# Performance work log

Hardware: AMD Instinct MI355X
Metric: run time of the kernel (lower is better)

## Reference

```python
import jax, jax.numpy as jnp
import numpy as np
import math

B, S, D, H = 2, 2048, 1024, 16
DH = D // H
MASK_VALUE = -1000000.0  # module uses -1e6, not -inf


def setup_inputs() -> dict:
    key = jax.random.key(0)
    ks = jax.random.split(key, 8)
    scale = 1.0 / math.sqrt(D)
    return {
        "queries": jax.random.normal(ks[0], (B, S, D), jnp.float32),
        "keys": jax.random.normal(ks[1], (B, S, D), jnp.float32),
        "values": jax.random.normal(ks[2], (B, S, D), jnp.float32),
        "valid_lens": jax.random.randint(ks[3], (B,), 1, S + 1, jnp.int32),
        "Wq": jax.random.normal(ks[4], (D, D), jnp.float32) * scale,
        "Wk": jax.random.normal(ks[5], (D, D), jnp.float32) * scale,
        "Wv": jax.random.normal(ks[6], (D, D), jnp.float32) * scale,
        "Wo": jax.random.normal(ks[7], (D, D), jnp.float32) * scale,
    }


def _split_heads(x):
    # [B, S, D] -> [B, H, S, DH]
    b, s, d = x.shape
    return x.reshape(b, s, H, DH).transpose(0, 2, 1, 3)


def reference(queries, keys, values, valid_lens, Wq, Wk, Wv, Wo):
    q = _split_heads(queries @ Wq)          # [B, H, S, DH]
    k = _split_heads(keys @ Wk)
    v = _split_heads(values @ Wv)
    scores = jnp.einsum("bhqd,bhkd->bhqk", q, k) / math.sqrt(DH)
    # valid_lens [B]: one length per batch row, broadcast over heads & queries
    mask = jnp.arange(scores.shape[-1])[None, None, None, :] < valid_lens[:, None, None, None]
    scores = jnp.where(mask, scores, MASK_VALUE)
    attn = jax.nn.softmax(scores, axis=-1)  # dropout is identity in eval
    out = jnp.einsum("bhqk,bhkd->bhqd", attn, v)   # [B, H, S, DH]
    out = out.transpose(0, 2, 1, 3).reshape(queries.shape[0], queries.shape[1], D)
    return out @ Wo
```

## Files before the change

### kernel.cpp

```cpp
#include <hip/hip_runtime.h>
#include <stdint.h>

#define BB 2
#define SS 2048
#define DD 1024
#define HH 16
#define DHD 64
#define MM (BB * SS)

typedef unsigned short u16;
typedef unsigned int u32;
typedef __attribute__((ext_vector_type(8))) short bhalf8;
typedef __attribute__((ext_vector_type(4))) float floatx4;
typedef __attribute__((ext_vector_type(2))) u32 u32x2;
typedef __attribute__((ext_vector_type(4))) u32 u32x4;
typedef __attribute__((address_space(3))) u32 as3_u32;
typedef __attribute__((address_space(1))) u32 as1_u32;

__device__ __forceinline__ u16 f2bf(float f) {
  u32 u = __float_as_uint(f);
  u32 r = (u + 0x7FFFu + ((u >> 16) & 1u)) >> 16;
  return (u16)r;
}

__device__ __forceinline__ u32 cvtpk_bf16(float lo, float hi) {
  u32 r;
  asm("v_cvt_pk_bf16_f32 %0, %1, %2" : "=v"(r) : "v"(lo), "v"(hi));
  return r;
}

__device__ __forceinline__ float exp2_fast(float x) {
  float r;
  asm("v_exp_f32 %0, %1" : "=v"(r) : "v"(x));
  return r;
}

__device__ __forceinline__ void gload16(const void* g, const void* l) {
  __builtin_amdgcn_global_load_lds((as1_u32*)(uintptr_t)g, (as3_u32*)(uintptr_t)l, 16, 0, 0);
}

__global__ void k_transpose4(const float* __restrict__ Wq, const float* __restrict__ Wk,
                             const float* __restrict__ Wv, const float* __restrict__ Wo,
                             u16* __restrict__ Wt) {
  const int z = blockIdx.z;
  const float* W = (z == 0) ? Wq : (z == 1) ? Wk : (z == 2) ? Wv : Wo;
  const float sc = (z == 0) ? 0.18033688011112042f : 1.0f;
  __shared__ u16 tile[32][33];
  const int tx = threadIdx.x, ty = threadIdx.y;
  const int n0 = blockIdx.x * 32, k0 = blockIdx.y * 32;
#pragma unroll
  for (int i = 0; i < 4; ++i)
    tile[ty + 8 * i][tx] = f2bf(W[(size_t)(k0 + ty + 8 * i) * DD + n0 + tx] * sc);
  __syncthreads();
  u16* dst = Wt + (size_t)z * 1048576;
#pragma unroll
  for (int i = 0; i < 4; ++i)
    dst[(size_t)(n0 + ty + 8 * i) * DD + k0 + tx] = tile[tx][ty + 8 * i];
}

__global__ __launch_bounds__(256, 2) void k_gemm_qkv(
    const float* __restrict__ Xq, const float* __restrict__ Xk, const float* __restrict__ Xv,
    const u16* __restrict__ Wt, u16* __restrict__ Qb, u16* __restrict__ Kb,
    u16* __restrict__ Vtb) {
  const int id = blockIdx.x;
  const int rr = id & 7, t8 = id >> 3;
  const int g = (t8 >> 3) * 8 + rr, c = t8 & 7;
  const int z = g / 32, by = g % 32, bx = c;
  const float* A = (z == 0) ? Xq : (z == 1) ? Xk : Xv;
  const u16* Bt = Wt + (size_t)z * 1048576;
  __shared__ __attribute__((aligned(16))) float sAf[2][128 * 32];
  __shared__ __attribute__((aligned(16))) u16 sB[2][128 * 32];
  const int t = threadIdx.x;
  const int w = t >> 6, lane = t & 63;
  const int lr = lane & 15, lg = lane >> 4;
  const int wr = w >> 1, wc = w & 1;
  const int row0 = by * 128, col0 = bx * 128;

  const int scol16 = (lane & 7) ^ (lane >> 3);
  const float* gA0 = A + (size_t)(row0 + w * 8 + (lane >> 3)) * DD + scol16 * 4;
  const int srowB = t >> 2;
  const int skoffB = (t & 3) * 8;
  const u16* gB = Bt + (size_t)(col0 + srowB) * DD + skoffB;
  const int ldsbaseB = w * 512;

  floatx4 acc[4][4] = {};

  auto stage = [&](int buf, int kt) {
    const int ko = kt * 32;
#pragma unroll
    for (int j = 0; j < 4; ++j)
      gload16(gA0 + (size_t)j * 32 * DD + ko, &sAf[buf][w * 256 + j * 1024]);
    gload16(gB + ko, &sB[buf][ldsbaseB]);
    gload16(gB + ko + (size_t)64 * DD, &sB[buf][2048 + ldsbaseB]);
  };

  const int swz = lr & 7;
  int cur = 0;
  stage(0, 0);
  __syncthreads();
  for (int kt = 0; kt < 32; ++kt) {
    if (kt + 1 < 32) stage(cur ^ 1, kt + 1);
    bhalf8 af[4], bf[4];
#pragma unroll
    for (int m = 0; m < 4; ++m) {
      const int r = wr * 64 + m * 16 + lr;
      const float4 a0 = *(const float4*)&sAf[cur][(r * 8 + ((lg * 2) ^ swz)) * 4];
      const float4 a1 = *(const float4*)&sAf[cur][(r * 8 + ((lg * 2 + 1) ^ swz)) * 4];
      u32x4 pk;
      pk.x = cvtpk_bf16(a0.x, a0.y); pk.y = cvtpk_bf16(a0.z, a0.w);
      pk.z = cvtpk_bf16(a1.x, a1.y); pk.w = cvtpk_bf16(a1.z, a1.w);
      af[m] = __builtin_bit_cast(bhalf8, pk);
    }
#pragma unroll
    for (int n = 0; n < 4; ++n)
      bf[n] = *(const bhalf8*)&sB[cur][(wc * 64 + n * 16 + lr) * 32 + lg * 8];
#pragma unroll
    for (int m = 0; m < 4; ++m)
#pragma unroll
      for (int n = 0; n < 4; ++n)
        acc[m][n] = __builtin_amdgcn_mfma_f32_16x16x32_bf16(af[m], bf[n], acc[m][n], 0, 0, 0);
    __syncthreads();
    cur ^= 1;
  }

#pragma unroll
  for (int m = 0; m < 4; ++m) {
#pragma unroll
    for (int n = 0; n < 4; ++n) {
      const int col = col0 + wc * 64 + n * 16 + lr;
      const int rowb = row0 + wr * 64 + m * 16 + lg * 4;
      if (z == 2) {
        const int bidx = rowb >> 11, s = rowb & (SS - 1);
        ushort4 pk;
        pk.x = f2bf(acc[m][n][0]); pk.y = f2bf(acc[m][n][1]);
        pk.z = f2bf(acc[m][n][2]); pk.w = f2bf(acc[m][n][3]);
        *(ushort4*)&Vtb[((size_t)bidx * 1024 + col) * SS + s] = pk;
      } else {
        u16* C = (z == 0) ? Qb : Kb;
#pragma unroll
        for (int r = 0; r < 4; ++r)
          C[(size_t)(rowb + r) * DD + col] = f2bf(acc[m][n][r]);
      }
    }
  }
}

template <int P>
__global__ __launch_bounds__(256, 2) void k_gemm_wo(
    const float* __restrict__ Opart, const float2* __restrict__ Ml,
    const int* __restrict__ valid_lens, const u16* __restrict__ Bt,
    float* __restrict__ C) {
  const int id = blockIdx.x;
  const int rr = id & 7, t8 = id >> 3;
  const int g = (t8 >> 3) * 8 + rr, c = t8 & 7;
  const int by = g, bx = c;
  __shared__ __attribute__((aligned(16))) u16 sA[2][64 * 32];
  __shared__ __attribute__((aligned(16))) u16 sB[2][128 * 32];
  const int t = threadIdx.x;
  const int w = t >> 6, lane = t & 63;
  const int lr = lane & 15, lg = lane >> 4;
  const int wr = w >> 1, wc = w & 1;
  const int row0 = by * 64, col0 = bx * 128;

  const int arow = t >> 2;
  const int R = row0 + arow;
  const int bb = R >> 11, s = R & (SS - 1);
  const int dcol = (t & 3) * 8;
  const bool live1 = (P == 2) && (valid_lens[bb] > SS / P);
  constexpr size_t PSTRIDE = (size_t)BB * HH * SS;

  const int srowB = t >> 2;
  const int skoffB = (t & 3) * 8;
  const u16* gB = Bt + (size_t)(col0 + srowB) * DD + skoffB;
  const int ldsbaseB = w * 512;

  floatx4 acc[2][4] = {};
  float4 x0, x1, y0, y1;
  float w0, w1;

  auto loadA = [&](int kt) {
    const int hh = kt >> 1, d0 = (kt & 1) * 32 + dcol;
    const size_t rbase = (size_t)(bb * HH + hh) * SS + s;
    x0 = *(const float4*)&Opart[rbase * DHD + d0];
    x1 = *(const float4*)&Opart[rbase * DHD + d0 + 4];
    const float2 ml0 = Ml[rbase];
    float L;
    if (live1) {
      const float2 ml1 = Ml[PSTRIDE + rbase];
      y0 = *(const float4*)&Opart[(PSTRIDE + rbase) * DHD + d0];
      y1 = *(const float4*)&Opart[(PSTRIDE + rbase) * DHD + d0 + 4];
      const float M = fmaxf(ml0.x, ml1.x);
      w0 = exp2_fast(ml0.x - M);
      w1 = exp2_fast(ml1.x - M);
      L = ml0.y * w0 + ml1.y * w1;
    } else {
      w0 = 1.f; w1 = 0.f;
      L = ml0.y;
    }
    const float inv = 1.0f / L;
    w0 *= inv; w1 *= inv;
  };

  auto writeA = [&](int buf) {
    float f0 = x0.x * w0, f1 = x0.y * w0, f2 = x0.z * w0, f3 = x0.w * w0;
    float f4 = x1.x * w0, f5 = x1.y * w0, f6 = x1.z * w0, f7 = x1.w * w0;
    if (live1) {
      f0 += y0.x * w1; f1 += y0.y * w1; f2 += y0.z * w1; f3 += y0.w * w1;
      f4 += y1.x * w1; f5 += y1.y * w1; f6 += y1.z * w1; f7 += y1.w * w1;
    }
    u32x4 pk;
    pk.x = cvtpk_bf16(f0, f1); pk.y = cvtpk_bf16(f2, f3);
    pk.z = cvtpk_bf16(f4, f5); pk.w = cvtpk_bf16(f6, f7);
    *(u32x4*)&sA[buf][arow * 32 + (t & 3) * 8] = pk;
  };

  auto stageB = [&](int buf, int kt) {
    const int ko = kt * 32;
    gload16(gB + ko, &sB[buf][ldsbaseB]);
    gload16(gB + ko + (size_t)64 * DD, &sB[buf][2048 + ldsbaseB]);
  };

  loadA(0);
  stageB(0, 0);
  writeA(0);
  __syncthreads();

  int cur = 0;
  for (int kt = 0; kt < 32; ++kt) {
    if (kt + 1 < 32) {
      stageB(cur ^ 1, kt + 1);
      loadA(kt + 1);
    }
    bhalf8 af[2], bf[4];
#pragma unroll
    for (int m = 0; m < 2; ++m)
      af[m] = *(const bhalf8*)&sA[cur][(wr * 32 + m * 16 + lr) * 32 + lg * 8];
#pragma unroll
    for (int n = 0; n < 4; ++n)
      bf[n] = *(const bhalf8*)&sB[cur][(wc * 64 + n * 16 + lr) * 32 + lg * 8];
#pragma unroll
    for (int m = 0; m < 2; ++m)
#pragma unroll
      for (int n = 0; n < 4; ++n)
        acc[m][n] = __builtin_amdgcn_mfma_f32_16x16x32_bf16(af[m], bf[n], acc[m][n], 0, 0, 0);
    if (kt + 1 < 32) writeA(cur ^ 1);
    __syncthreads();
    cur ^= 1;
  }

#pragma unroll
  for (int m = 0; m < 2; ++m)
#pragma unroll
    for (int n = 0; n < 4; ++n) {
      const int col = col0 + wc * 64 + n * 16 + lr;
      const int rowb = row0 + wr * 32 + m * 16 + lg * 4;
#pragma unroll
      for (int r = 0; r < 4; ++r)
        C[(size_t)(rowb + r) * DD + col] = acc[m][n][r];
    }
}

__global__ __launch_bounds__(256, 2) void k_attn(
    const u16* __restrict__ Q, const u16* __restrict__ K, const u16* __restrict__ Vt,
    float* __restrict__ Opart, float2* __restrict__ Ml,
    const int* __restrict__ valid_lens, const int part) {
  const int id = blockIdx.x;
  const int rr = id & 7, tt = id >> 3;
  const int g = (tt >> 5) * 8 + rr, c = tt & 31;
  const int h = g & 15, zi = g >> 4;
  const int b = zi & 1, p = zi >> 1;
  const int t = threadIdx.x;
  const int w = t >> 6, lane = t & 63;
  const int lr = lane & 15, lg = lane >> 4;
  const int q0 = c * 64 + w * 16;
  const int vl = valid_lens[b];
  const int kbeg = p * part;
  if (kbeg >= vl) return;
  const int kend = (vl < kbeg + part) ? vl : (kbeg + part);
  const int L = kend - kbeg;

  __shared__ __attribute__((aligned(16))) u16 kbuf[2][64 * 64];
  __shared__ __attribute__((aligned(16))) u16 vbuf[2][64 * 64];
  __shared__ __attribute__((aligned(16))) u16 p_lds[4][16 * 72];
  u16* pl = &p_lds[w][0];

  const u16* Qp = Q + ((size_t)(b * SS + q0 + lr)) * DD + h * DHD;
  const bhalf8 qf0 = *(const bhalf8*)(Qp + lg * 8);
  const bhalf8 qf1 = *(const bhalf8*)(Qp + 32 + lg * 8);

  const int sub = lane >> 3;
  const int sc16 = (lane & 7) ^ sub;
  const u16* ksrc = K + (size_t)(b * SS + kbeg + w * 16 + sub) * DD + h * DHD + sc16 * 8;
  const u16* vsrc = Vt + ((size_t)(b * HH + h) * DHD + w * 16 + sub) * SS + kbeg + sc16 * 8;

  auto stage = [&](int buf, int i) {
    const int sk0 = i * 64;
    gload16(ksrc + (size_t)sk0 * DD,       &kbuf[buf][(w * 16) * 64]);
    gload16(ksrc + (size_t)(sk0 + 8) * DD, &kbuf[buf][(w * 16 + 8) * 64]);
    gload16(vsrc + sk0,                    &vbuf[buf][(w * 16) * 64]);
    gload16(vsrc + (size_t)8 * SS + sk0,   &vbuf[buf][(w * 16 + 8) * 64]);
  };

  float mrun = -1e30f, lrun = 0.f;
  floatx4 o[4] = {};

  const int nblk = (L + 63) >> 6;
  const bool partial = (L & 63) != 0;
  const int swz = lr & 7;

  stage(0, 0);
  __syncthreads();

  int cb = 0;
  for (int i = 0; i < nblk; ++i) {
    if (i + 1 < nblk) stage(cb ^ 1, i + 1);
    const u16* kb = &kbuf[cb][0];
    const u16* vb = &vbuf[cb][0];
    floatx4 s[4];
    __builtin_amdgcn_s_setprio(1);
#pragma unroll
    for (int cc = 0; cc < 4; ++cc) {
      const bhalf8 kc0 = *(const bhalf8*)&kb[(cc * 16 + lr) * 64 + ((lg ^ swz) * 8)];
      const bhalf8 kc1 = *(const bhalf8*)&kb[(cc * 16 + lr) * 64 + (((lg + 4) ^ swz) * 8)];
      floatx4 zz = {0.f, 0.f, 0.f, 0.f};
      zz = __builtin_amdgcn_mfma_f32_16x16x32_bf16(kc0, qf0, zz, 0, 0, 0);
      s[cc] = __builtin_amdgcn_mfma_f32_16x16x32_bf16(kc1, qf1, zz, 0, 0, 0);
    }
    __builtin_amdgcn_s_setprio(0);
    if (partial && i == nblk - 1) {
      const int sk0 = i * 64;
#pragma unroll
      for (int cc = 0; cc < 4; ++cc)
#pragma unroll
        for (int r = 0; r < 4; ++r)
          if (sk0 + cc * 16 + lg * 4 + r >= L) s[cc][r] = -1e6f;
    }
    float tmax = fmaxf(fmaxf(fmaxf(s[0][0], s[0][1]), fmaxf(s[0][2], s[0][3])),
                       fmaxf(fmaxf(s[1][0], s[1][1]), fmaxf(s[1][2], s[1][3])));
    tmax = fmaxf(tmax, fmaxf(fmaxf(fmaxf(s[2][0], s[2][1]), fmaxf(s[2][2], s[2][3])),
                             fmaxf(fmaxf(s[3][0], s[3][1]), fmaxf(s[3][2], s[3][3]))));
    tmax = fmaxf(tmax, __shfl_xor(tmax, 16));
    tmax = fmaxf(tmax, __shfl_xor(tmax, 32));
    if (!__all(tmax <= mrun + 8.0f)) {
      const float nm = fmaxf(mrun, tmax);
      const float sc = exp2_fast(mrun - nm);
      mrun = nm;
      lrun *= sc;
      float scb[4];
#pragma unroll
      for (int r = 0; r < 4; ++r) scb[r] = __shfl(sc, lg * 4 + r);
#pragma unroll
      for (int dt = 0; dt < 4; ++dt)
#pragma unroll
        for (int r = 0; r < 4; ++r) o[dt][r] *= scb[r];
    }
    float rs = 0.f;
    u32 pk[4][2];
#pragma unroll
    for (int cc = 0; cc < 4; ++cc) {
      float p0 = exp2_fast(s[cc][0] - mrun), p1 = exp2_fast(s[cc][1] - mrun);
      float p2 = exp2_fast(s[cc][2] - mrun), p3 = exp2_fast(s[cc][3] - mrun);
      rs += (p0 + p1) + (p2 + p3);
      pk[cc][0] = cvtpk_bf16(p0, p1);
      pk[cc][1] = cvtpk_bf16(p2, p3);
    }
    rs += __shfl_xor(rs, 16);
    rs += __shfl_xor(rs, 32);
    lrun += rs;
#pragma unroll
    for (int cc = 0; cc < 4; ++cc) {
      u32x2 pr; pr.x = pk[cc][0]; pr.y = pk[cc][1];
      *(u32x2*)&pl[lr * 72 + cc * 16 + lg * 4] = pr;
    }
    asm volatile("s_waitcnt lgkmcnt(0)" ::: "memory");
    const bhalf8 pa0 = *(const bhalf8*)&pl[lr * 72 + lg * 8];
    const bhalf8 pa1 = *(const bhalf8*)&pl[lr * 72 + 32 + lg * 8];
    __builtin_amdgcn_s_setprio(1);
#pragma unroll
    for (int dt = 0; dt < 4; ++dt) {
      const bhalf8 vf0 = *(const bhalf8*)&vb[(dt * 16 + lr) * 64 + ((lg ^ swz) * 8)];
      const bhalf8 vf1 = *(const bhalf8*)&vb[(dt * 16 + lr) * 64 + (((lg + 4) ^ swz) * 8)];
      o[dt] = __builtin_amdgcn_mfma_f32_16x16x32_bf16(pa0, vf0, o[dt], 0, 0, 0);
      o[dt] = __builtin_amdgcn_mfma_f32_16x16x32_bf16(pa1, vf1, o[dt], 0, 0, 0);
    }
    __builtin_amdgcn_s_setprio(0);
    __syncthreads();
    cb ^= 1;
  }

  const size_t rowbase = ((size_t)(b * HH + h)) * SS + q0;
  const size_t pbase = (size_t)p * (BB * HH * SS);
#pragma unroll
  for (int dt = 0; dt < 4; ++dt)
#pragma unroll
    for (int r = 0; r < 4; ++r)
      Opart[(pbase + rowbase + lg * 4 + r) * DHD + dt * 16 + lr] = o[dt][r];
  if (lane < 16) {
    float2 ml; ml.x = mrun; ml.y = lrun;
    Ml[pbase + rowbase + lr] = ml;
  }
}

extern "C" void kernel_launch(void* const* d_in, const int* in_sizes, int n_in,
                              void* d_out, int out_size, void* d_ws, size_t ws_size,
                              hipStream_t stream) {
  const float* q = (const float*)d_in[0];
  const float* k = (const float*)d_in[1];
  const float* v = (const float*)d_in[2];
  const int* vl = (const int*)d_in[3];
  const float* Wq = (const float*)d_in[4];
  const float* Wk = (const float*)d_in[5];
  const float* Wv = (const float*)d_in[6];
  const float* Wo = (const float*)d_in[7];

  char* ws = (char*)d_ws;
  u16* Wt  = (u16*)(ws + 0);
  u16* Qb  = (u16*)(ws + 8388608);
  u16* Kb  = (u16*)(ws + 16777216);
  u16* Vtb = (u16*)(ws + 25165824);
  float* Opart = (float*)(ws + 33554432);

  const bool big = ws_size >= (size_t)134 * 1024 * 1024;
  const int P = big ? 2 : 1;
  const int part = SS / P;
  float2* Ml = big ? (float2*)(ws + 67108864) : (float2*)(ws + 50331648);

  k_transpose4<<<dim3(32, 32, 4), dim3(32, 8), 0, stream>>>(Wq, Wk, Wv, Wo, Wt);
  k_gemm_qkv<<<768, 256, 0, stream>>>(q, k, v, Wt, Qb, Kb, Vtb);
  k_attn<<<1024 * P, 256, 0, stream>>>(Qb, Kb, Vtb, Opart, Ml, vl, part);
  u16* Wto = Wt + 3 * 1048576;
  if (big) k_gemm_wo<2><<<512, 256, 0, stream>>>(Opart, Ml, vl, Wto, (float*)d_out);
  else     k_gemm_wo<1><<<512, 256, 0, stream>>>(Opart, Ml, vl, Wto, (float*)d_out);
}
```

Baseline: 228.6 us.

## Pre-convert QKV activations to bf16 in a separate kernel before projection GEMM

```diff
diff --git a/kernel.cpp b/kernel.cpp
--- a/kernel.cpp
+++ b/kernel.cpp
@@ -37,6 +37,17 @@
 
 __device__ __forceinline__ void gload16(const void* g, const void* l) {
   __builtin_amdgcn_global_load_lds((as1_u32*)(uintptr_t)g, (as3_u32*)(uintptr_t)l, 16, 0, 0);
+}
+
+__global__ void k_convert3(const float* __restrict__ q, const float* __restrict__ k,
+                           const float* __restrict__ v, u16* __restrict__ out) {
+  const int z = blockIdx.y;
+  const float* src = (z == 0) ? q : (z == 1) ? k : v;
+  const int i = blockIdx.x * 256 + threadIdx.x;
+  float4 val = ((const float4*)src)[i];
+  ushort4 o;
+  o.x = f2bf(val.x); o.y = f2bf(val.y); o.z = f2bf(val.z); o.w = f2bf(val.w);
+  ((ushort4*)(out + (size_t)z * 4194304))[i] = o;
 }
 
 __global__ void k_transpose4(const float* __restrict__ Wq, const float* __restrict__ Wk,
@@ -59,16 +70,16 @@
 }
 
 __global__ __launch_bounds__(256, 2) void k_gemm_qkv(
-    const float* __restrict__ Xq, const float* __restrict__ Xk, const float* __restrict__ Xv,
+    const u16* __restrict__ Xq, const u16* __restrict__ Xk, const u16* __restrict__ Xv,
     const u16* __restrict__ Wt, u16* __restrict__ Qb, u16* __restrict__ Kb,
     u16* __restrict__ Vtb) {
   const int id = blockIdx.x;
   const int rr = id & 7, t8 = id >> 3;
   const int g = (t8 >> 3) * 8 + rr, c = t8 & 7;
   const int z = g / 32, by = g % 32, bx = c;
-  const float* A = (z == 0) ? Xq : (z == 1) ? Xk : Xv;
+  const u16* A = (z == 0) ? Xq : (z == 1) ? Xk : Xv;
   const u16* Bt = Wt + (size_t)z * 1048576;
-  __shared__ __attribute__((aligned(16))) float sAf[2][128 * 32];
+  __shared__ __attribute__((aligned(16))) u16 sA[2][128 * 32];
   __shared__ __attribute__((aligned(16))) u16 sB[2][128 * 32];
   const int t = threadIdx.x;
   const int w = t >> 6, lane = t & 63;
@@ -76,25 +87,22 @@
   const int wr = w >> 1, wc = w & 1;
   const int row0 = by * 128, col0 = bx * 128;
 
-  const int scol16 = (lane & 7) ^ (lane >> 3);
-  const float* gA0 = A + (size_t)(row0 + w * 8 + (lane >> 3)) * DD + scol16 * 4;
-  const int srowB = t >> 2;
-  const int skoffB = (t & 3) * 8;
-  const u16* gB = Bt + (size_t)(col0 + srowB) * DD + skoffB;
-  const int ldsbaseB = w * 512;
+  const int srow = t >> 2;
+  const int skoff = (t & 3) * 8;
+  const u16* gA = A + (size_t)(row0 + srow) * DD + skoff;
+  const u16* gB = Bt + (size_t)(col0 + srow) * DD + skoff;
+  const int ldsbase = w * 512;
 
   floatx4 acc[4][4] = {};
 
   auto stage = [&](int buf, int kt) {
     const int ko = kt * 32;
-#pragma unroll
-    for (int j = 0; j < 4; ++j)
-      gload16(gA0 + (size_t)j * 32 * DD + ko, &sAf[buf][w * 256 + j * 1024]);
-    gload16(gB + ko, &sB[buf][ldsbaseB]);
-    gload16(gB + ko + (size_t)64 * DD, &sB[buf][2048 + ldsbaseB]);
+    gload16(gA + ko, &sA[buf][ldsbase]);
+    gload16(gA + ko + (size_t)64 * DD, &sA[buf][2048 + ldsbase]);
+    gload16(gB + ko, &sB[buf][ldsbase]);
+    gload16(gB + ko + (size_t)64 * DD, &sB[buf][2048 + ldsbase]);
   };
 
-  const int swz = lr & 7;
   int cur = 0;
   stage(0, 0);
   __syncthreads();
@@ -102,15 +110,8 @@
     if (kt + 1 < 32) stage(cur ^ 1, kt + 1);
     bhalf8 af[4], bf[4];
 #pragma unroll
-    for (int m = 0; m < 4; ++m) {
-      const int r = wr * 64 + m * 16 + lr;
-      const float4 a0 = *(const float4*)&sAf[cur][(r * 8 + ((lg * 2) ^ swz)) * 4];
-      const float4 a1 = *(const float4*)&sAf[cur][(r * 8 + ((lg * 2 + 1) ^ swz)) * 4];
-      u32x4 pk;
-      pk.x = cvtpk_bf16(a0.x, a0.y); pk.y = cvtpk_bf16(a0.z, a0.w);
-      pk.z = cvtpk_bf16(a1.x, a1.y); pk.w = cvtpk_bf16(a1.z, a1.w);
-      af[m] = __builtin_bit_cast(bhalf8, pk);
-    }
+    for (int m = 0; m < 4; ++m)
+      af[m] = *(const bhalf8*)&sA[cur][(wr * 64 + m * 16 + lr) * 32 + lg * 8];
 #pragma unroll
     for (int n = 0; n < 4; ++n)
       bf[n] = *(const bhalf8*)&sB[cur][(wc * 64 + n * 16 + lr) * 32 + lg * 8];
@@ -260,7 +261,7 @@
     }
 }
 
-__global__ __launch_bounds__(256, 2) void k_attn(
+__global__ __launch_bounds__(256, 3) void k_attn(
     const u16* __restrict__ Q, const u16* __restrict__ K, const u16* __restrict__ Vt,
     float* __restrict__ Opart, float2* __restrict__ Ml,
     const int* __restrict__ valid_lens, const int part) {
@@ -414,19 +415,21 @@
   const float* Wo = (const float*)d_in[7];
 
   char* ws = (char*)d_ws;
-  u16* Wt  = (u16*)(ws + 0);
-  u16* Qb  = (u16*)(ws + 8388608);
-  u16* Kb  = (u16*)(ws + 16777216);
-  u16* Vtb = (u16*)(ws + 25165824);
-  float* Opart = (float*)(ws + 33554432);
+  u16* Xq  = (u16*)(ws + 0);
+  u16* Wt  = (u16*)(ws + 25165824);
+  u16* Qb  = (u16*)(ws + 33554432);
+  u16* Kb  = (u16*)(ws + 41943040);
+  u16* Vtb = (u16*)(ws + 50331648);
 
   const bool big = ws_size >= (size_t)134 * 1024 * 1024;
   const int P = big ? 2 : 1;
   const int part = SS / P;
-  float2* Ml = big ? (float2*)(ws + 67108864) : (float2*)(ws + 50331648);
-
+  float* Opart = big ? (float*)(ws + 67108864) : (float*)(ws + 0);
+  float2* Ml   = big ? (float2*)(ws + 100663296) : (float2*)(ws + 16777216);
+
+  k_convert3<<<dim3(4096, 3), 256, 0, stream>>>(q, k, v, Xq);
   k_transpose4<<<dim3(32, 32, 4), dim3(32, 8), 0, stream>>>(Wq, Wk, Wv, Wo, Wt);
-  k_gemm_qkv<<<768, 256, 0, stream>>>(q, k, v, Wt, Qb, Kb, Vtb);
+  k_gemm_qkv<<<768, 256, 0, stream>>>(Xq, Xq + 4194304, Xq + 8388608, Wt, Qb, Kb, Vtb);
   k_attn<<<1024 * P, 256, 0, stream>>>(Qb, Kb, Vtb, Opart, Ml, vl, part);
   u16* Wto = Wt + 3 * 1048576;
   if (big) k_gemm_wo<2><<<512, 256, 0, stream>>>(Opart, Ml, vl, Wto, (float*)d_out);
```

New measurement: 219.5 us. 4.0% less time.
